# Kernel optimization log

Measured on AMD Instinct MI355X. Metric: run time of the kernel, lower is better.

## Reference

```python
import jax, jax.numpy as jnp
import numpy as np

B, N, D, H, R, K = 64, 197, 768, 3072, 16, 1


def setup_inputs() -> dict:
    key = jax.random.key(0)
    ks = jax.random.split(key, 9)
    s1 = 1.0 / np.sqrt(D)
    s2 = 1.0 / np.sqrt(H)
    return {
        "x": jax.random.normal(ks[0], (B, N, D), dtype=jnp.float32),
        "W1": jax.random.normal(ks[1], (H, D), dtype=jnp.float32) * s1,
        "b1": jax.random.normal(ks[2], (H,), dtype=jnp.float32) * s1,
        "A1": jax.random.normal(ks[3], (K, R, D), dtype=jnp.float32) * s1,
        "B1": jax.random.normal(ks[4], (K, H, R), dtype=jnp.float32) * 0.01,
        "W2": jax.random.normal(ks[5], (D, H), dtype=jnp.float32) * s2,
        "b2": jax.random.normal(ks[6], (D,), dtype=jnp.float32) * s2,
        "A2": jax.random.normal(ks[7], (K, R, H), dtype=jnp.float32) * s2,
        "B2": jax.random.normal(ks[8], (K, D, R), dtype=jnp.float32) * 0.01,
    }


def _lora(x, A, Bm):
    # result of torch: (B @ (A @ x^T.unsqueeze(1))).sum(1).transpose(1,2)
    # A: [K, r, d_in], Bm: [K, d_out, r], x: [b, n, d_in] -> [b, n, d_out]
    t = jnp.einsum('krd,bnd->bknr', A, x)          # low-rank projection
    return jnp.einsum('kor,bknr->bno', Bm, t)      # expand + sum over K


def reference(x, W1, b1, A1, B1, W2, b2, A2, B2):
    # fc1 (Linear + LoRA correction)
    h = jnp.einsum('bnd,hd->bnh', x, W1) + b1 + _lora(x, A1, B1)
    # exact (erf-based) GELU, matching torch nn.GELU default
    h = jax.nn.gelu(h, approximate=False)
    # dropout p=0 and norm=Identity by default -> no-ops
    out = jnp.einsum('bnh,dh->bnd', h, W2) + b2 + _lora(h, A2, B2)
    return out
```

## Files before the change

kernel.cpp:

```cpp
#include <hip/hip_runtime.h>
#include <math.h>

#define M_ROWS 12608
#define D_DIM  768
#define H_DIM  3072

typedef __bf16 bf16_t;
typedef __bf16 bf16x8 __attribute__((ext_vector_type(8)));
typedef float  f32x4  __attribute__((ext_vector_type(4)));

__device__ __forceinline__ void gl2lds16(const bf16_t* g, bf16_t* l) {
  __builtin_amdgcn_global_load_lds(
      (__attribute__((address_space(1))) void*)g,
      (__attribute__((address_space(3))) void*)l,
      16, 0, 0);
}

__device__ __forceinline__ float gelu_fast(float v) {
  float xs = v * 0.70710678118654752f;
  float ax = fabsf(xs);
  float t = __builtin_amdgcn_rcpf(1.0f + 0.3275911f * ax);
  float poly = t * (0.254829592f +
              t * (-0.284496736f +
              t * (1.421413741f +
              t * (-1.453152027f +
              t * 1.061405429f))));
  float er = 1.0f - poly * __expf(-ax * ax);
  er = (xs < 0.0f) ? -er : er;
  return 0.5f * v * (1.0f + er);
}

__global__ void cast_f32_bf16_kernel(const float* __restrict__ in,
                                     bf16_t* __restrict__ out, long n) {
  long i = ((long)blockIdx.x * 256 + threadIdx.x) * 4;
  if (i + 3 < n) {
    float4 v = *(const float4*)(in + i);
    out[i + 0] = (bf16_t)v.x; out[i + 1] = (bf16_t)v.y;
    out[i + 2] = (bf16_t)v.z; out[i + 3] = (bf16_t)v.w;
  } else {
    for (; i < n; ++i) out[i] = (bf16_t)in[i];
  }
}

__global__ void fold_lora_kernel(const float* __restrict__ W,
                                 const float* __restrict__ A,
                                 const float* __restrict__ Bm,
                                 bf16_t* __restrict__ Weff,
                                 int OUT, int IN) {
  long idx = (long)blockIdx.x * 256 + threadIdx.x;
  if (idx >= (long)OUT * IN) return;
  int o = (int)(idx / IN);
  int i = (int)(idx - (long)o * IN);
  float s = W[idx];
#pragma unroll
  for (int r = 0; r < 16; ++r)
    s += Bm[o * 16 + r] * A[r * IN + i];
  Weff[idx] = (bf16_t)s;
}

__global__ __launch_bounds__(256, 2) void gemm1_kernel(
    const bf16_t* __restrict__ Amat, const bf16_t* __restrict__ Bmat,
    const float* __restrict__ bias, bf16_t* __restrict__ Cmat,
    int Mrows, int Ncols, int Kd) {
  __shared__ char smem[24576];
  bf16_t* sA = (bf16_t*)smem;
  bf16_t* sB = (bf16_t*)(smem + 16384);
  float*  sT = (float*)smem;

  const int tid = threadIdx.x, lane = tid & 63, wave = tid >> 6;
  const int wm = wave & 1, wn = wave >> 1;
  const int row0 = blockIdx.y * 256, col0 = blockIdx.x * 128;

  const bf16_t* gA[4]; const bf16_t* gB[2];
  bf16_t* lA[4]; bf16_t* lB[2];
#pragma unroll
  for (int q = 0; q < 4; ++q) {
    int c = tid + q * 256;
    int r = c >> 2;
    int kcg = (c & 3) ^ ((r >> 1) & 3);
    int ra = row0 + r; if (ra > Mrows - 1) ra = Mrows - 1;
    gA[q] = Amat + (size_t)ra * Kd + kcg * 8;
    lA[q] = sA + (q * 256 + wave * 64) * 8;
  }
#pragma unroll
  for (int q = 0; q < 2; ++q) {
    int c = tid + q * 256;
    int r = c >> 2;
    int kcg = (c & 3) ^ ((r >> 1) & 3);
    gB[q] = Bmat + (size_t)(col0 + r) * Kd + kcg * 8;
    lB[q] = sB + (q * 256 + wave * 64) * 8;
  }

  const int rl = lane & 15, kc = lane >> 4;
  int aoffs[8], boffs[4];
#pragma unroll
  for (int i = 0; i < 8; ++i) {
    int r = wm * 128 + i * 16 + rl;
    aoffs[i] = r * 32 + ((kc ^ ((r >> 1) & 3)) * 8);
  }
#pragma unroll
  for (int j = 0; j < 4; ++j) {
    int r = wn * 64 + j * 16 + rl;
    boffs[j] = r * 32 + ((kc ^ ((r >> 1) & 3)) * 8);
  }

  f32x4 acc[8][4] = {};
  const int iters = Kd / 32;
  for (int it = 0; it < iters; ++it) {
#pragma unroll
    for (int q = 0; q < 4; ++q) gl2lds16(gA[q], lA[q]);
#pragma unroll
    for (int q = 0; q < 2; ++q) gl2lds16(gB[q], lB[q]);
#pragma unroll
    for (int q = 0; q < 4; ++q) gA[q] += 32;
#pragma unroll
    for (int q = 0; q < 2; ++q) gB[q] += 32;
    __syncthreads();

    bf16x8 af[8], bfr[4];
#pragma unroll
    for (int i = 0; i < 8; ++i) af[i] = *(const bf16x8*)(sA + aoffs[i]);
#pragma unroll
    for (int j = 0; j < 4; ++j) bfr[j] = *(const bf16x8*)(sB + boffs[j]);
#pragma unroll
    for (int i = 0; i < 8; ++i)
#pragma unroll
      for (int j = 0; j < 4; ++j)
        acc[i][j] = __builtin_amdgcn_mfma_f32_16x16x32_bf16(
            af[i], bfr[j], acc[i][j], 0, 0, 0);
    __syncthreads();
  }

  const int crow = (lane >> 4) * 4, ccol = lane & 15;
  const int erow = tid >> 3, eseg = tid & 7;
#pragma unroll
  for (int mi = 0; mi < 8; ++mi) {
#pragma unroll
    for (int ni = 0; ni < 4; ++ni)
#pragma unroll
      for (int r = 0; r < 4; ++r)
        sT[(wm * 16 + crow + r) * 132 + wn * 64 + ni * 16 + ccol] = acc[mi][ni][r];
    __syncthreads();
    const int grow = row0 + (erow >> 4) * 128 + mi * 16 + (erow & 15);
    if (grow < Mrows) {
      const float* src = sT + erow * 132 + eseg * 16;
      bf16_t ov[16];
#pragma unroll
      for (int p = 0; p < 16; ++p) {
        float v = src[p] + bias[col0 + eseg * 16 + p];
        ov[p] = (bf16_t)gelu_fast(v);
      }
      bf16_t* dst = Cmat + (size_t)grow * Ncols + col0 + eseg * 16;
      *(bf16x8*)dst = *(bf16x8*)ov;
      *(bf16x8*)(dst + 8) = *(bf16x8*)(ov + 8);
    }
    __syncthreads();
  }
}

__global__ __launch_bounds__(256) void gemm2_kernel(
    const bf16_t* __restrict__ Amat, const bf16_t* __restrict__ Bmat,
    const float* __restrict__ bias, float* __restrict__ Cmat,
    int Mrows, int Ncols, int Kd) {
  __shared__ bf16_t sA[128 * 32];
  __shared__ bf16_t sB[128 * 32];
  const int tid = threadIdx.x, lane = tid & 63, wave = tid >> 6;
  const int wm = wave & 1, wn = wave >> 1;
  const int row0 = blockIdx.y * 128, col0 = blockIdx.x * 128;

  const bf16_t* gA[2]; const bf16_t* gB[2];
  bf16_t* lA[2]; bf16_t* lB[2];
#pragma unroll
  for (int q = 0; q < 2; ++q) {
    int c = tid + q * 256;
    int r = c >> 2;
    int kcg = (c & 3) ^ ((r >> 1) & 3);
    int ra = row0 + r; if (ra > Mrows - 1) ra = Mrows - 1;
    gA[q] = Amat + (size_t)ra * Kd + kcg * 8;
    lA[q] = sA + (q * 256 + wave * 64) * 8;
    gB[q] = Bmat + (size_t)(col0 + r) * Kd + kcg * 8;
    lB[q] = sB + (q * 256 + wave * 64) * 8;
  }

  const int rl = lane & 15, kc = lane >> 4;
  int aoffs[4], boffs[4];
#pragma unroll
  for (int i = 0; i < 4; ++i) {
    int ra = wm * 64 + i * 16 + rl;
    int rb = wn * 64 + i * 16 + rl;
    aoffs[i] = ra * 32 + ((kc ^ ((ra >> 1) & 3)) * 8);
    boffs[i] = rb * 32 + ((kc ^ ((rb >> 1) & 3)) * 8);
  }

  f32x4 acc[4][4] = {};
  const int iters = Kd / 32;
  for (int it = 0; it < iters; ++it) {
#pragma unroll
    for (int q = 0; q < 2; ++q) gl2lds16(gA[q], lA[q]);
#pragma unroll
    for (int q = 0; q < 2; ++q) gl2lds16(gB[q], lB[q]);
#pragma unroll
    for (int q = 0; q < 2; ++q) { gA[q] += 32; gB[q] += 32; }
    __syncthreads();

    bf16x8 af[4], bfr[4];
#pragma unroll
    for (int i = 0; i < 4; ++i) af[i] = *(const bf16x8*)(sA + aoffs[i]);
#pragma unroll
    for (int i = 0; i < 4; ++i) bfr[i] = *(const bf16x8*)(sB + boffs[i]);
#pragma unroll
    for (int mi = 0; mi < 4; ++mi)
#pragma unroll
      for (int ni = 0; ni < 4; ++ni)
        acc[mi][ni] = __builtin_amdgcn_mfma_f32_16x16x32_bf16(
            af[mi], bfr[ni], acc[mi][ni], 0, 0, 0);
    __syncthreads();
  }

  const int crow = (lane >> 4) * 4, ccol = lane & 15;
#pragma unroll
  for (int ni = 0; ni < 4; ++ni) {
    const int gc = col0 + wn * 64 + ni * 16 + ccol;
    const float bv = bias[gc];
#pragma unroll
    for (int mi = 0; mi < 4; ++mi) {
      const int gr = row0 + wm * 64 + mi * 16 + crow;
#pragma unroll
      for (int r = 0; r < 4; ++r) {
        const int row = gr + r;
        if (row < Mrows)
          Cmat[(size_t)row * Ncols + gc] = acc[mi][ni][r] + bv;
      }
    }
  }
}

extern "C" void kernel_launch(void* const* d_in, const int* in_sizes, int n_in,
                              void* d_out, int out_size, void* d_ws, size_t ws_size,
                              hipStream_t stream) {
  const float* x  = (const float*)d_in[0];
  const float* W1 = (const float*)d_in[1];
  const float* b1 = (const float*)d_in[2];
  const float* A1 = (const float*)d_in[3];
  const float* B1 = (const float*)d_in[4];
  const float* W2 = (const float*)d_in[5];
  const float* b2 = (const float*)d_in[6];
  const float* A2 = (const float*)d_in[7];
  const float* B2 = (const float*)d_in[8];
  float* out = (float*)d_out;

  char* ws = (char*)d_ws;
  bf16_t* xb    = (bf16_t*)ws;
  bf16_t* W1eff = (bf16_t*)(ws + 19366144);
  bf16_t* W2eff = (bf16_t*)(ws + 19366144 + 4718592);
  bf16_t* hbuf  = (bf16_t*)(ws + 19366144 + 2 * 4718592);

  const long nx = (long)M_ROWS * D_DIM;
  cast_f32_bf16_kernel<<<(int)((nx / 4 + 255) / 256), 256, 0, stream>>>(x, xb, nx);

  const int foldBlocks = (H_DIM * D_DIM + 255) / 256;
  fold_lora_kernel<<<foldBlocks, 256, 0, stream>>>(W1, A1, B1, W1eff, H_DIM, D_DIM);
  fold_lora_kernel<<<foldBlocks, 256, 0, stream>>>(W2, A2, B2, W2eff, D_DIM, H_DIM);

  gemm1_kernel<<<dim3(H_DIM / 128, (M_ROWS + 255) / 256), 256, 0, stream>>>(
      xb, W1eff, b1, hbuf, M_ROWS, H_DIM, D_DIM);
  gemm2_kernel<<<dim3(D_DIM / 128, (M_ROWS + 127) / 128), 256, 0, stream>>>(
      hbuf, W2eff, b2, out, M_ROWS, D_DIM, H_DIM);
}
```

Before: 341.9 us.

## Double the K-step to 64 in both GEMMs and add XCD-aware block swizzle

Both GEMM kernels now stage 64-wide K slices in LDS instead of 32, with a new XOR swizzle for 8 chunks per row. This halves the number of barrier pairs per tile. Launches become 1D grids that map consecutive block IDs to row bands spread across the 8 XCDs, so blocks sharing weight columns land on the same XCD's L2. The larger LDS footprint in gemm1 (48KB) may limit occupancy to fewer blocks per CU.

```diff
diff --git a/kernel.cpp b/kernel.cpp
--- a/kernel.cpp
+++ b/kernel.cpp
@@ -62,32 +62,40 @@
     const bf16_t* __restrict__ Amat, const bf16_t* __restrict__ Bmat,
     const float* __restrict__ bias, bf16_t* __restrict__ Cmat,
     int Mrows, int Ncols, int Kd) {
-  __shared__ char smem[24576];
+  __shared__ char smem[49152];
   bf16_t* sA = (bf16_t*)smem;
-  bf16_t* sB = (bf16_t*)(smem + 16384);
+  bf16_t* sB = (bf16_t*)(smem + 32768);
   float*  sT = (float*)smem;
+
+  {
+  }
+  const int gswz = blockIdx.x;
+  const int xcd = gswz & 7, tswz = gswz >> 3;
+  const int colb = tswz % 24, rband = tswz / 24;
+  const int rowb = rband * 8 + xcd;
+  if (rowb >= 50) return;
+  const int row0 = rowb * 256, col0 = colb * 128;
 
   const int tid = threadIdx.x, lane = tid & 63, wave = tid >> 6;
   const int wm = wave & 1, wn = wave >> 1;
-  const int row0 = blockIdx.y * 256, col0 = blockIdx.x * 128;
-
-  const bf16_t* gA[4]; const bf16_t* gB[2];
-  bf16_t* lA[4]; bf16_t* lB[2];
+
+  const bf16_t* gA[8]; const bf16_t* gB[4];
+  bf16_t* lA[8]; bf16_t* lB[4];
+#pragma unroll
+  for (int q = 0; q < 8; ++q) {
+    int c = tid + q * 256;
+    int r = c >> 3;
+    int kkg = (c & 7) ^ (r & 7);
+    int ra = row0 + r; if (ra > Mrows - 1) ra = Mrows - 1;
+    gA[q] = Amat + (size_t)ra * Kd + kkg * 8;
+    lA[q] = sA + (q * 256 + wave * 64) * 8;
+  }
 #pragma unroll
   for (int q = 0; q < 4; ++q) {
     int c = tid + q * 256;
-    int r = c >> 2;
-    int kcg = (c & 3) ^ ((r >> 1) & 3);
-    int ra = row0 + r; if (ra > Mrows - 1) ra = Mrows - 1;
-    gA[q] = Amat + (size_t)ra * Kd + kcg * 8;
-    lA[q] = sA + (q * 256 + wave * 64) * 8;
-  }
-#pragma unroll
-  for (int q = 0; q < 2; ++q) {
-    int c = tid + q * 256;
-    int r = c >> 2;
-    int kcg = (c & 3) ^ ((r >> 1) & 3);
-    gB[q] = Bmat + (size_t)(col0 + r) * Kd + kcg * 8;
+    int r = c >> 3;
+    int kkg = (c & 7) ^ (r & 7);
+    gB[q] = Bmat + (size_t)(col0 + r) * Kd + kkg * 8;
     lB[q] = sB + (q * 256 + wave * 64) * 8;
   }
 
@@ -96,38 +104,41 @@
 #pragma unroll
   for (int i = 0; i < 8; ++i) {
     int r = wm * 128 + i * 16 + rl;
-    aoffs[i] = r * 32 + ((kc ^ ((r >> 1) & 3)) * 8);
+    aoffs[i] = r * 64 + ((kc ^ (r & 3)) + ((r >> 2) & 1) * 4) * 8;
   }
 #pragma unroll
   for (int j = 0; j < 4; ++j) {
     int r = wn * 64 + j * 16 + rl;
-    boffs[j] = r * 32 + ((kc ^ ((r >> 1) & 3)) * 8);
+    boffs[j] = r * 64 + ((kc ^ (r & 3)) + ((r >> 2) & 1) * 4) * 8;
   }
 
   f32x4 acc[8][4] = {};
-  const int iters = Kd / 32;
+  const int iters = Kd / 64;
   for (int it = 0; it < iters; ++it) {
 #pragma unroll
-    for (int q = 0; q < 4; ++q) gl2lds16(gA[q], lA[q]);
-#pragma unroll
-    for (int q = 0; q < 2; ++q) gl2lds16(gB[q], lB[q]);
-#pragma unroll
-    for (int q = 0; q < 4; ++q) gA[q] += 32;
-#pragma unroll
-    for (int q = 0; q < 2; ++q) gB[q] += 32;
-    __syncthreads();
-
-    bf16x8 af[8], bfr[4];
-#pragma unroll
-    for (int i = 0; i < 8; ++i) af[i] = *(const bf16x8*)(sA + aoffs[i]);
-#pragma unroll
-    for (int j = 0; j < 4; ++j) bfr[j] = *(const bf16x8*)(sB + boffs[j]);
-#pragma unroll
-    for (int i = 0; i < 8; ++i)
-#pragma unroll
-      for (int j = 0; j < 4; ++j)
-        acc[i][j] = __builtin_amdgcn_mfma_f32_16x16x32_bf16(
-            af[i], bfr[j], acc[i][j], 0, 0, 0);
+    for (int q = 0; q < 8; ++q) gl2lds16(gA[q], lA[q]);
+#pragma unroll
+    for (int q = 0; q < 4; ++q) gl2lds16(gB[q], lB[q]);
+#pragma unroll
+    for (int q = 0; q < 8; ++q) gA[q] += 64;
+#pragma unroll
+    for (int q = 0; q < 4; ++q) gB[q] += 64;
+    __syncthreads();
+
+#pragma unroll
+    for (int ks = 0; ks < 2; ++ks) {
+      bf16x8 af[8], bfr[4];
+#pragma unroll
+      for (int i = 0; i < 8; ++i) af[i] = *(const bf16x8*)(sA + (aoffs[i] ^ (ks * 32)));
+#pragma unroll
+      for (int j = 0; j < 4; ++j) bfr[j] = *(const bf16x8*)(sB + (boffs[j] ^ (ks * 32)));
+#pragma unroll
+      for (int i = 0; i < 8; ++i)
+#pragma unroll
+        for (int j = 0; j < 4; ++j)
+          acc[i][j] = __builtin_amdgcn_mfma_f32_16x16x32_bf16(
+              af[i], bfr[j], acc[i][j], 0, 0, 0);
+    }
     __syncthreads();
   }
 
@@ -162,23 +173,30 @@
     const bf16_t* __restrict__ Amat, const bf16_t* __restrict__ Bmat,
     const float* __restrict__ bias, float* __restrict__ Cmat,
     int Mrows, int Ncols, int Kd) {
-  __shared__ bf16_t sA[128 * 32];
-  __shared__ bf16_t sB[128 * 32];
+  __shared__ bf16_t sA[128 * 64];
+  __shared__ bf16_t sB[128 * 64];
+
+  const int gswz = blockIdx.x;
+  const int xcd = gswz & 7, tswz = gswz >> 3;
+  const int colb = tswz % 6, rband = tswz / 6;
+  const int rowb = rband * 8 + xcd;
+  if (rowb >= 99) return;
+  const int row0 = rowb * 128, col0 = colb * 128;
+
   const int tid = threadIdx.x, lane = tid & 63, wave = tid >> 6;
   const int wm = wave & 1, wn = wave >> 1;
-  const int row0 = blockIdx.y * 128, col0 = blockIdx.x * 128;
-
-  const bf16_t* gA[2]; const bf16_t* gB[2];
-  bf16_t* lA[2]; bf16_t* lB[2];
-#pragma unroll
-  for (int q = 0; q < 2; ++q) {
+
+  const bf16_t* gA[4]; const bf16_t* gB[4];
+  bf16_t* lA[4]; bf16_t* lB[4];
+#pragma unroll
+  for (int q = 0; q < 4; ++q) {
     int c = tid + q * 256;
-    int r = c >> 2;
-    int kcg = (c & 3) ^ ((r >> 1) & 3);
+    int r = c >> 3;
+    int kkg = (c & 7) ^ (r & 7);
     int ra = row0 + r; if (ra > Mrows - 1) ra = Mrows - 1;
-    gA[q] = Amat + (size_t)ra * Kd + kcg * 8;
+    gA[q] = Amat + (size_t)ra * Kd + kkg * 8;
     lA[q] = sA + (q * 256 + wave * 64) * 8;
-    gB[q] = Bmat + (size_t)(col0 + r) * Kd + kcg * 8;
+    gB[q] = Bmat + (size_t)(col0 + r) * Kd + kkg * 8;
     lB[q] = sB + (q * 256 + wave * 64) * 8;
   }
 
@@ -188,32 +206,35 @@
   for (int i = 0; i < 4; ++i) {
     int ra = wm * 64 + i * 16 + rl;
     int rb = wn * 64 + i * 16 + rl;
-    aoffs[i] = ra * 32 + ((kc ^ ((ra >> 1) & 3)) * 8);
-    boffs[i] = rb * 32 + ((kc ^ ((rb >> 1) & 3)) * 8);
+    aoffs[i] = ra * 64 + ((kc ^ (ra & 3)) + ((ra >> 2) & 1) * 4) * 8;
+    boffs[i] = rb * 64 + ((kc ^ (rb & 3)) + ((rb >> 2) & 1) * 4) * 8;
   }
 
   f32x4 acc[4][4] = {};
-  const int iters = Kd / 32;
+  const int iters = Kd / 64;
   for (int it = 0; it < iters; ++it) {
 #pragma unroll
-    for (int q = 0; q < 2; ++q) gl2lds16(gA[q], lA[q]);
-#pragma unroll
-    for (int q = 0; q < 2; ++q) gl2lds16(gB[q], lB[q]);
-#pragma unroll
-    for (int q = 0; q < 2; ++q) { gA[q] += 32; gB[q] += 32; }
-    __syncthreads();
-
-    bf16x8 af[4], bfr[4];
-#pragma unroll
-    for (int i = 0; i < 4; ++i) af[i] = *(const bf16x8*)(sA + aoffs[i]);
-#pragma unroll
-    for (int i = 0; i < 4; ++i) bfr[i] = *(const bf16x8*)(sB + boffs[i]);
-#pragma unroll
-    for (int mi = 0; mi < 4; ++mi)
-#pragma unroll
-      for (int ni = 0; ni < 4; ++ni)
-        acc[mi][ni] = __builtin_amdgcn_mfma_f32_16x16x32_bf16(
-            af[mi], bfr[ni], acc[mi][ni], 0, 0, 0);
+    for (int q = 0; q < 4; ++q) gl2lds16(gA[q], lA[q]);
+#pragma unroll
+    for (int q = 0; q < 4; ++q) gl2lds16(gB[q], lB[q]);
+#pragma unroll
+    for (int q = 0; q < 4; ++q) { gA[q] += 64; gB[q] += 64; }
+    __syncthreads();
+
+#pragma unroll
+    for (int ks = 0; ks < 2; ++ks) {
+      bf16x8 af[4], bfr[4];
+#pragma unroll
+      for (int i = 0; i < 4; ++i) af[i] = *(const bf16x8*)(sA + (aoffs[i] ^ (ks * 32)));
+#pragma unroll
+      for (int i = 0; i < 4; ++i) bfr[i] = *(const bf16x8*)(sB + (boffs[i] ^ (ks * 32)));
+#pragma unroll
+      for (int mi = 0; mi < 4; ++mi)
+#pragma unroll
+        for (int ni = 0; ni < 4; ++ni)
+          acc[mi][ni] = __builtin_amdgcn_mfma_f32_16x16x32_bf16(
+              af[mi], bfr[ni], acc[mi][ni], 0, 0, 0);
+    }
     __syncthreads();
   }
 
@@ -262,8 +283,6 @@
   fold_lora_kernel<<<foldBlocks, 256, 0, stream>>>(W1, A1, B1, W1eff, H_DIM, D_DIM);
   fold_lora_kernel<<<foldBlocks, 256, 0, stream>>>(W2, A2, B2, W2eff, D_DIM, H_DIM);
 
-  gemm1_kernel<<<dim3(H_DIM / 128, (M_ROWS + 255) / 256), 256, 0, stream>>>(
-      xb, W1eff, b1, hbuf, M_ROWS, H_DIM, D_DIM);
-  gemm2_kernel<<<dim3(D_DIM / 128, (M_ROWS + 127) / 128), 256, 0, stream>>>(
-      hbuf, W2eff, b2, out, M_ROWS, D_DIM, H_DIM);
-}
+  gemm1_kernel<<<1344, 256, 0, stream>>>(xb, W1eff, b1, hbuf, M_ROWS, H_DIM, D_DIM);
+  gemm2_kernel<<<624, 256, 0, stream>>>(hbuf, W2eff, b2, out, M_ROWS, D_DIM, H_DIM);
+}
```

Result: faster. 302.3 us (-11.6%).
